# Kernel optimization log

Hardware: AMD Instinct MI355X
Metric: run time of the kernel (lower is better)

## Reference

```python
import jax, jax.numpy as jnp
import numpy as np


def setup_inputs() -> dict:
    key = jax.random.key(0)
    kq, kk, kv = jax.random.split(key, 3)
    B, S, D = 4, 4096, 64
    return {
        "q": jax.random.normal(kq, (B, S, D), dtype=jnp.float32),
        "k": jax.random.normal(kk, (B, S, D), dtype=jnp.float32),
        "v": jax.random.normal(kv, (B, S, D), dtype=jnp.float32),
    }


def reference(q, k, v):
    B, S, D = q.shape
    scale = 1.0 / jnp.sqrt(jnp.asarray(D, dtype=q.dtype))
    # (B, S, S) full score matrix, as in the naive torch implementation
    scores = jnp.einsum("bqd,bkd->bqk", q, k) * scale
    causal_mask = jnp.tril(jnp.ones((S, S), dtype=bool))  # True = keep
    scores = jnp.where(causal_mask, scores, -jnp.inf)
    attn = jax.nn.softmax(scores, axis=-1)
    return jnp.einsum("bqk,bkd->bqd", attn, v)
```

## Files before the change

### kernel.cpp

```cpp
#include <hip/hip_runtime.h>
#include <hip/hip_bf16.h>

typedef __bf16 bf16x8 __attribute__((ext_vector_type(8)));
typedef __bf16 bf16x4 __attribute__((ext_vector_type(4)));
typedef float  floatx4 __attribute__((ext_vector_type(4)));

#define SD 4096
#define DH 64
#define NB 4

__device__ __forceinline__ float exp2fast(float x) { return __builtin_amdgcn_exp2f(x); }

__device__ __forceinline__ unsigned pack_bf16_2(float a, float b) {
    union { __bf16 h[2]; unsigned u; } cvt;
    cvt.h[0] = (__bf16)a; cvt.h[1] = (__bf16)b;
    return cvt.u;
}

__device__ __forceinline__ void block_sync_lds() {
    asm volatile("s_waitcnt lgkmcnt(0)\n\ts_barrier" ::: "memory");
}

__global__ __launch_bounds__(256) void prep_kernel(const float* __restrict__ v,
                                                   __bf16* __restrict__ vt) {
    __shared__ __bf16 tile[16][80];
    const int bid = blockIdx.x;
    const int tid = threadIdx.x;
    const int b = bid >> 8, kt = (bid >> 2) & 63, dq = bid & 3;
    {
        int key = tid >> 2, ds = (tid & 3) * 4;
        float4 f = *(const float4*)(v + ((long)b * SD + kt * 64 + key) * DH + dq * 16 + ds);
        tile[ds+0][key] = (__bf16)f.x;
        tile[ds+1][key] = (__bf16)f.y;
        tile[ds+2][key] = (__bf16)f.z;
        tile[ds+3][key] = (__bf16)f.w;
    }
    __syncthreads();
    {
        int dloc = tid >> 4, cs = (tid & 15) * 4;
        bf16x4 o;
#pragma unroll
        for (int i = 0; i < 4; ++i) {
            int col = cs + i;
            int key = ((col >> 5) * 2 + ((col >> 2) & 1)) * 16
                    + ((col >> 3) & 3) * 4 + (col & 3);
            o[i] = tile[dloc][key];
        }
        *(bf16x4*)(vt + ((long)b * DH + dq * 16 + dloc) * SD + kt * 64 + cs) = o;
    }
}

__global__ __launch_bounds__(256, 4) void fa_kernel(const float* __restrict__ q,
                                                    const float* __restrict__ kq,
                                                    const __bf16* __restrict__ vt,
                                                    __bf16* __restrict__ opart,
                                                    float* __restrict__ lpart) {
    __shared__ __bf16 smem[2][8192];

    const int tid  = threadIdx.x;
    const int wave = tid >> 6;
    const int lane = tid & 63;
    const int c    = lane & 15;
    const int quad = lane >> 4;
    const int bid   = blockIdx.x;
    const int batch = bid & 3;
    const int pr    = (bid >> 2) & 31;
    const int qr    = bid >> 7;
    const float sc = 0.125f * 1.4426950408889634f;

    const long offB   = (long)batch * SD * DH;
    const long vtoffB = (long)batch * DH * SD;

    const int krow = tid >> 2, kdc = (tid & 3) * 16;
    auto swz = [](int g) { int row = g >> 3, ch = g & 7; return row * 64 + ((ch ^ (row & 7)) << 3); };
    const int wkA = swz(krow * 8 + (tid & 3) * 2);
    const int wkB = swz(krow * 8 + (tid & 3) * 2 + 1);
    const int gk0 = tid, gk1 = tid + 256;
    const int wv0 = 4096 + swz(gk0), wv1 = 4096 + swz(gk1);
    const int sw   = c & 7;
    const int off0 = ((quad ^ sw) << 3);
    const int off1 = (((quad + 4) ^ sw) << 3);
    const int rowc = c * 64;

#pragma unroll 1
    for (int ph = 0; ph < 2; ++ph) {
        const int T = ph ? 63 - pr : pr;
        const int myq = T * 64 + wave * 16;
        const int qrow = myq + c;

        bf16x8 qf0, qf1;
        {
            const float* qp = q + offB + (long)(myq + c) * DH + quad * 8;
            float4 f0 = *(const float4*)(qp);
            float4 f1 = *(const float4*)(qp + 4);
            float4 f2 = *(const float4*)(qp + 32);
            float4 f3 = *(const float4*)(qp + 36);
            qf0[0]=(__bf16)(f0.x*sc); qf0[1]=(__bf16)(f0.y*sc); qf0[2]=(__bf16)(f0.z*sc); qf0[3]=(__bf16)(f0.w*sc);
            qf0[4]=(__bf16)(f1.x*sc); qf0[5]=(__bf16)(f1.y*sc); qf0[6]=(__bf16)(f1.z*sc); qf0[7]=(__bf16)(f1.w*sc);
            qf1[0]=(__bf16)(f2.x*sc); qf1[1]=(__bf16)(f2.y*sc); qf1[2]=(__bf16)(f2.z*sc); qf1[3]=(__bf16)(f2.w*sc);
            qf1[4]=(__bf16)(f3.x*sc); qf1[5]=(__bf16)(f3.y*sc); qf1[6]=(__bf16)(f3.z*sc); qf1[7]=(__bf16)(f3.w*sc);
        }

        floatx4 o0 = {0.f,0.f,0.f,0.f}, o1 = o0, o2 = o0, o3 = o0;
        float l = 0.0f;

        const int n = (T >= qr) ? ((T - qr) >> 3) + 1 : 0;

        float4 fk0, fk1, fk2, fk3;
        bf16x8 sv0, sv1;
        auto stage = [&](int kt, float4& a0, float4& a1, float4& a2, float4& a3,
                         bf16x8& v0, bf16x8& v1) {
            const float* kg = kq + offB + (long)(kt * 64 + krow) * DH + kdc;
            a0 = *(const float4*)(kg);
            a1 = *(const float4*)(kg + 4);
            a2 = *(const float4*)(kg + 8);
            a3 = *(const float4*)(kg + 12);
            const __bf16* vg = vt + vtoffB + kt * 64;
            v0 = *(const bf16x8*)(vg + (long)(gk0 >> 3) * SD + (gk0 & 7) * 8);
            v1 = *(const bf16x8*)(vg + (long)(gk1 >> 3) * SD + (gk1 & 7) * 8);
        };

        if (n > 0) stage(qr, fk0, fk1, fk2, fk3, sv0, sv1);
        block_sync_lds();

#pragma unroll 1
        for (int j = 0; j < n; ++j) {
            const int kt = qr + 8 * j;
            float4 nk0, nk1, nk2, nk3; bf16x8 nv0, nv1;
            if (j + 1 < n) stage(kt + 8, nk0, nk1, nk2, nk3, nv0, nv1);
            __bf16* buf = smem[j & 1];
            {
                bf16x8 cA, cB;
                cA[0]=(__bf16)fk0.x; cA[1]=(__bf16)fk0.y; cA[2]=(__bf16)fk0.z; cA[3]=(__bf16)fk0.w;
                cA[4]=(__bf16)fk1.x; cA[5]=(__bf16)fk1.y; cA[6]=(__bf16)fk1.z; cA[7]=(__bf16)fk1.w;
                cB[0]=(__bf16)fk2.x; cB[1]=(__bf16)fk2.y; cB[2]=(__bf16)fk2.z; cB[3]=(__bf16)fk2.w;
                cB[4]=(__bf16)fk3.x; cB[5]=(__bf16)fk3.y; cB[6]=(__bf16)fk3.z; cB[7]=(__bf16)fk3.w;
                *(bf16x8*)(buf + wkA) = cA;
                *(bf16x8*)(buf + wkB) = cB;
                *(bf16x8*)(buf + wv0) = sv0;
                *(bf16x8*)(buf + wv1) = sv1;
            }
            fk0 = nk0; fk1 = nk1; fk2 = nk2; fk3 = nk3; sv0 = nv0; sv1 = nv1;
            block_sync_lds();

            const int kbase = kt * 64;
            if (kbase > myq + 15) continue;

            const __bf16* kbuf = buf;
            const __bf16* vbuf = buf + 4096;
            floatx4 sa[4];
#pragma unroll
            for (int t = 0; t < 4; ++t) {
                bf16x8 ka  = *(const bf16x8*)(kbuf + t * 1024 + rowc + off0);
                bf16x8 kb2 = *(const bf16x8*)(kbuf + t * 1024 + rowc + off1);
                floatx4 a = {0.f,0.f,0.f,0.f};
                a = __builtin_amdgcn_mfma_f32_16x16x32_bf16(ka,  qf0, a, 0, 0, 0);
                a = __builtin_amdgcn_mfma_f32_16x16x32_bf16(kb2, qf1, a, 0, 0, 0);
                sa[t] = a;
            }
            float pe[16];
            if (kbase + 63 > myq) {
#pragma unroll
                for (int t = 0; t < 4; ++t)
#pragma unroll
                    for (int r = 0; r < 4; ++r) {
                        int key = kbase + t*16 + quad*4 + r;
                        pe[t*4+r] = (key <= qrow) ? exp2fast(sa[t][r]) : 0.0f;
                    }
            } else {
#pragma unroll
                for (int t = 0; t < 4; ++t)
#pragma unroll
                    for (int r = 0; r < 4; ++r) pe[t*4+r] = exp2fast(sa[t][r]);
            }
            {
                float s8[8], s4v[4];
#pragma unroll
                for (int i = 0; i < 8; ++i) s8[i] = pe[i] + pe[i+8];
#pragma unroll
                for (int i = 0; i < 4; ++i) s4v[i] = s8[i] + s8[i+4];
                l += (s4v[0] + s4v[2]) + (s4v[1] + s4v[3]);
            }
#pragma unroll
            for (int s = 0; s < 2; ++s) {
                union { unsigned u[4]; bf16x8 f; } bp;
#pragma unroll
                for (int jj = 0; jj < 4; ++jj)
                    bp.u[jj] = pack_bf16_2(pe[8*s + 2*jj], pe[8*s + 2*jj + 1]);
                const int offs = s ? off1 : off0;
                bf16x8 v0 = *(const bf16x8*)(vbuf + 0*1024 + rowc + offs);
                bf16x8 v1 = *(const bf16x8*)(vbuf + 1*1024 + rowc + offs);
                bf16x8 v2 = *(const bf16x8*)(vbuf + 2*1024 + rowc + offs);
                bf16x8 v3 = *(const bf16x8*)(vbuf + 3*1024 + rowc + offs);
                o0 = __builtin_amdgcn_mfma_f32_16x16x32_bf16(v0, bp.f, o0, 0, 0, 0);
                o1 = __builtin_amdgcn_mfma_f32_16x16x32_bf16(v1, bp.f, o1, 0, 0, 0);
                o2 = __builtin_amdgcn_mfma_f32_16x16x32_bf16(v2, bp.f, o2, 0, 0, 0);
                o3 = __builtin_amdgcn_mfma_f32_16x16x32_bf16(v3, bp.f, o3, 0, 0, 0);
            }
        }

        l += __shfl_xor(l, 16);
        l += __shfl_xor(l, 32);

        __bf16* ob = opart + ((long)qr * NB + batch) * (long)(SD * DH) + (long)myq * DH;
        {
            floatx4 ov[4] = {o0, o1, o2, o3};
#pragma unroll
            for (int dt = 0; dt < 4; ++dt) {
                uint2 sO;
                sO.x = pack_bf16_2(ov[dt][0], ov[dt][1]);
                sO.y = pack_bf16_2(ov[dt][2], ov[dt][3]);
                *(uint2*)(ob + c * DH + dt*16 + quad*4) = sO;
            }
        }
        if (quad == 0)
            lpart[((long)qr * NB + batch) * SD + myq + c] = l;
    }
}

__global__ __launch_bounds__(256) void combine_kernel(const __bf16* __restrict__ opart,
                                                      const float* __restrict__ lpart,
                                                      float* __restrict__ out) {
    const long t    = (long)blockIdx.x * 256 + threadIdx.x;
    const long base = t * 4;
    const long qq   = base >> 6;
    float n0 = 0.f, n1 = 0.f, n2 = 0.f, n3 = 0.f, den = 0.f;
#pragma unroll
    for (int qr = 0; qr < 8; ++qr) {
        bf16x4 p = *(const bf16x4*)(opart + ((long)qr << 20) + base);
        n0 += (float)p[0]; n1 += (float)p[1]; n2 += (float)p[2]; n3 += (float)p[3];
        den += lpart[((long)qr << 14) + qq];
    }
    float inv = 1.0f / den;
    float4 o; o.x = n0 * inv; o.y = n1 * inv; o.z = n2 * inv; o.w = n3 * inv;
    *(float4*)(out + base) = o;
}

extern "C" void kernel_launch(void* const* d_in, const int* in_sizes, int n_in,
                              void* d_out, int out_size, void* d_ws, size_t ws_size,
                              hipStream_t stream) {
    const float* q = (const float*)d_in[0];
    const float* k = (const float*)d_in[1];
    const float* v = (const float*)d_in[2];
    float* out = (float*)d_out;
    __bf16* vtb   = (__bf16*)d_ws;
    __bf16* opart = (__bf16*)((char*)d_ws + (4u << 20));
    float*  lpart = (float*)((char*)d_ws + (20u << 20));
    prep_kernel<<<dim3(1024), dim3(256), 0, stream>>>(v, vtb);
    fa_kernel<<<dim3(1024), dim3(256), 0, stream>>>(q, k, vtb, opart, lpart);
    combine_kernel<<<dim3(1024), dim3(256), 0, stream>>>(opart, lpart, out);
}
```

Measured before the change: 94.23 us.

## Stage 128-key tiles per iteration and halve the split-K partition count

Each loop iteration now stages two 64-key K/V sub-tiles (128 keys) into a doubled shared buffer and runs the score/PV body twice per barrier. The key dimension is split into 4 partitions instead of 8, so the attention grid drops to 512 blocks and the combine kernel reads half as many partial outputs. The aim is fewer barriers per key processed and less partial-result traffic. The cost is more registers and LDS per block (occupancy bound lowered to 2) and fewer blocks to spread over the CUs, which may hurt load balance under the causal mask.

```diff
diff --git a/kernel.cpp b/kernel.cpp
--- a/kernel.cpp
+++ b/kernel.cpp
@@ -50,12 +50,12 @@
     }
 }
 
-__global__ __launch_bounds__(256, 4) void fa_kernel(const float* __restrict__ q,
+__global__ __launch_bounds__(256, 2) void fa_kernel(const float* __restrict__ q,
                                                     const float* __restrict__ kq,
                                                     const __bf16* __restrict__ vt,
                                                     __bf16* __restrict__ opart,
                                                     float* __restrict__ lpart) {
-    __shared__ __bf16 smem[2][8192];
+    __shared__ __bf16 smem[2][16384];
 
     const int tid  = threadIdx.x;
     const int wave = tid >> 6;
@@ -73,10 +73,10 @@
 
     const int krow = tid >> 2, kdc = (tid & 3) * 16;
     auto swz = [](int g) { int row = g >> 3, ch = g & 7; return row * 64 + ((ch ^ (row & 7)) << 3); };
-    const int wkA = swz(krow * 8 + (tid & 3) * 2);
-    const int wkB = swz(krow * 8 + (tid & 3) * 2 + 1);
+    const int kg0 = krow * 8 + (tid & 3) * 2;
+    const int wkA = swz(kg0), wkB = swz(kg0 + 1);
     const int gk0 = tid, gk1 = tid + 256;
-    const int wv0 = 4096 + swz(gk0), wv1 = 4096 + swz(gk1);
+    const int wva = swz(gk0), wvb = swz(gk1);
     const int sw   = c & 7;
     const int off0 = ((quad ^ sw) << 3);
     const int off1 = (((quad + 4) ^ sw) << 3);
@@ -104,50 +104,27 @@
         floatx4 o0 = {0.f,0.f,0.f,0.f}, o1 = o0, o2 = o0, o3 = o0;
         float l = 0.0f;
 
-        const int n = (T >= qr) ? ((T - qr) >> 3) + 1 : 0;
-
-        float4 fk0, fk1, fk2, fk3;
-        bf16x8 sv0, sv1;
-        auto stage = [&](int kt, float4& a0, float4& a1, float4& a2, float4& a3,
-                         bf16x8& v0, bf16x8& v1) {
-            const float* kg = kq + offB + (long)(kt * 64 + krow) * DH + kdc;
-            a0 = *(const float4*)(kg);
-            a1 = *(const float4*)(kg + 4);
-            a2 = *(const float4*)(kg + 8);
-            a3 = *(const float4*)(kg + 12);
-            const __bf16* vg = vt + vtoffB + kt * 64;
-            v0 = *(const bf16x8*)(vg + (long)(gk0 >> 3) * SD + (gk0 & 7) * 8);
-            v1 = *(const bf16x8*)(vg + (long)(gk1 >> 3) * SD + (gk1 & 7) * 8);
+        const int last = T >> 1;
+        const int n = (last >= qr) ? ((last - qr) >> 2) + 1 : 0;
+
+        float4 fk[8];
+        bf16x8 sv[4];
+        auto stage = [&](int kt, float4* a, bf16x8* vv) {
+            const float* kg = kq + offB + (long)(kt * 128 + krow) * DH + kdc;
+#pragma unroll
+            for (int i = 0; i < 4; ++i) {
+                a[i]     = *(const float4*)(kg + i * 4);
+                a[i + 4] = *(const float4*)(kg + 64 * DH + i * 4);
+            }
+            const __bf16* vg = vt + vtoffB + kt * 128;
+            vv[0] = *(const bf16x8*)(vg + (long)(gk0 >> 3) * SD + (gk0 & 7) * 8);
+            vv[1] = *(const bf16x8*)(vg + (long)(gk1 >> 3) * SD + (gk1 & 7) * 8);
+            vv[2] = *(const bf16x8*)(vg + (long)(gk0 >> 3) * SD + 64 + (gk0 & 7) * 8);
+            vv[3] = *(const bf16x8*)(vg + (long)(gk1 >> 3) * SD + 64 + (gk1 & 7) * 8);
         };
 
-        if (n > 0) stage(qr, fk0, fk1, fk2, fk3, sv0, sv1);
-        block_sync_lds();
-
-#pragma unroll 1
-        for (int j = 0; j < n; ++j) {
-            const int kt = qr + 8 * j;
-            float4 nk0, nk1, nk2, nk3; bf16x8 nv0, nv1;
-            if (j + 1 < n) stage(kt + 8, nk0, nk1, nk2, nk3, nv0, nv1);
-            __bf16* buf = smem[j & 1];
-            {
-                bf16x8 cA, cB;
-                cA[0]=(__bf16)fk0.x; cA[1]=(__bf16)fk0.y; cA[2]=(__bf16)fk0.z; cA[3]=(__bf16)fk0.w;
-                cA[4]=(__bf16)fk1.x; cA[5]=(__bf16)fk1.y; cA[6]=(__bf16)fk1.z; cA[7]=(__bf16)fk1.w;
-                cB[0]=(__bf16)fk2.x; cB[1]=(__bf16)fk2.y; cB[2]=(__bf16)fk2.z; cB[3]=(__bf16)fk2.w;
-                cB[4]=(__bf16)fk3.x; cB[5]=(__bf16)fk3.y; cB[6]=(__bf16)fk3.z; cB[7]=(__bf16)fk3.w;
-                *(bf16x8*)(buf + wkA) = cA;
-                *(bf16x8*)(buf + wkB) = cB;
-                *(bf16x8*)(buf + wv0) = sv0;
-                *(bf16x8*)(buf + wv1) = sv1;
-            }
-            fk0 = nk0; fk1 = nk1; fk2 = nk2; fk3 = nk3; sv0 = nv0; sv1 = nv1;
-            block_sync_lds();
-
-            const int kbase = kt * 64;
-            if (kbase > myq + 15) continue;
-
-            const __bf16* kbuf = buf;
-            const __bf16* vbuf = buf + 4096;
+        auto body = [&](const __bf16* kbuf, const __bf16* vbuf, int kb) {
+            if (kb > myq + 15) return;
             floatx4 sa[4];
 #pragma unroll
             for (int t = 0; t < 4; ++t) {
@@ -159,12 +136,12 @@
                 sa[t] = a;
             }
             float pe[16];
-            if (kbase + 63 > myq) {
+            if (kb + 63 > myq) {
 #pragma unroll
                 for (int t = 0; t < 4; ++t)
 #pragma unroll
                     for (int r = 0; r < 4; ++r) {
-                        int key = kbase + t*16 + quad*4 + r;
+                        int key = kb + t*16 + quad*4 + r;
                         pe[t*4+r] = (key <= qrow) ? exp2fast(sa[t][r]) : 0.0f;
                     }
             } else {
@@ -197,6 +174,38 @@
                 o2 = __builtin_amdgcn_mfma_f32_16x16x32_bf16(v2, bp.f, o2, 0, 0, 0);
                 o3 = __builtin_amdgcn_mfma_f32_16x16x32_bf16(v3, bp.f, o3, 0, 0, 0);
             }
+        };
+
+        if (n > 0) stage(qr, fk, sv);
+        block_sync_lds();
+
+#pragma unroll 1
+        for (int j = 0; j < n; ++j) {
+            const int kt = qr + 4 * j;
+            float4 nk[8]; bf16x8 nv[4];
+            if (j + 1 < n) stage(kt + 4, nk, nv);
+            __bf16* buf = smem[j & 1];
+#pragma unroll
+            for (int h = 0; h < 2; ++h) {
+                bf16x8 cA, cB;
+                const float4 a0 = fk[h*4+0], a1 = fk[h*4+1], a2 = fk[h*4+2], a3 = fk[h*4+3];
+                cA[0]=(__bf16)a0.x; cA[1]=(__bf16)a0.y; cA[2]=(__bf16)a0.z; cA[3]=(__bf16)a0.w;
+                cA[4]=(__bf16)a1.x; cA[5]=(__bf16)a1.y; cA[6]=(__bf16)a1.z; cA[7]=(__bf16)a1.w;
+                cB[0]=(__bf16)a2.x; cB[1]=(__bf16)a2.y; cB[2]=(__bf16)a2.z; cB[3]=(__bf16)a2.w;
+                cB[4]=(__bf16)a3.x; cB[5]=(__bf16)a3.y; cB[6]=(__bf16)a3.z; cB[7]=(__bf16)a3.w;
+                *(bf16x8*)(buf + h*4096 + wkA) = cA;
+                *(bf16x8*)(buf + h*4096 + wkB) = cB;
+                *(bf16x8*)(buf + 8192 + h*4096 + wva) = sv[h*2+0];
+                *(bf16x8*)(buf + 8192 + h*4096 + wvb) = sv[h*2+1];
+            }
+#pragma unroll
+            for (int i = 0; i < 8; ++i) fk[i] = nk[i];
+#pragma unroll
+            for (int i = 0; i < 4; ++i) sv[i] = nv[i];
+            block_sync_lds();
+
+            body(buf,        buf + 8192,  kt * 128);
+            body(buf + 4096, buf + 12288, kt * 128 + 64);
         }
 
         l += __shfl_xor(l, 16);
@@ -226,7 +235,7 @@
     const long qq   = base >> 6;
     float n0 = 0.f, n1 = 0.f, n2 = 0.f, n3 = 0.f, den = 0.f;
 #pragma unroll
-    for (int qr = 0; qr < 8; ++qr) {
+    for (int qr = 0; qr < 4; ++qr) {
         bf16x4 p = *(const bf16x4*)(opart + ((long)qr << 20) + base);
         n0 += (float)p[0]; n1 += (float)p[1]; n2 += (float)p[2]; n3 += (float)p[3];
         den += lpart[((long)qr << 14) + qq];
@@ -245,8 +254,8 @@
     float* out = (float*)d_out;
     __bf16* vtb   = (__bf16*)d_ws;
     __bf16* opart = (__bf16*)((char*)d_ws + (4u << 20));
-    float*  lpart = (float*)((char*)d_ws + (20u << 20));
+    float*  lpart = (float*)((char*)d_ws + (16u << 20));
     prep_kernel<<<dim3(1024), dim3(256), 0, stream>>>(v, vtb);
-    fa_kernel<<<dim3(1024), dim3(256), 0, stream>>>(q, k, vtb, opart, lpart);
+    fa_kernel<<<dim3(512), dim3(256), 0, stream>>>(q, k, vtb, opart, lpart);
     combine_kernel<<<dim3(1024), dim3(256), 0, stream>>>(opart, lpart, out);
 }
```

After: 93.69 us. Within noise of the previous version (-0.6%).

## Pre-swizzle K/V to bf16 tiles and stage via direct global-to-LDS loads

Applied to the files above, without the earlier changes.

The prep kernel now converts K to bf16 and lays out both K and transposed V as pre-swizzled 64x64 tiles. The attention kernel then copies each tile straight into LDS with global_load_lds, with no register round trip. This removes the per-iteration fp32-to-bf16 conversion of K, the register staging and the LDS stores from the main loop, and halves K read traffic. The cost is extra prep work and a barrier that waits on all outstanding loads, which could expose load latency because prefetch now issues after the barrier.

```diff
diff --git a/kernel.cpp b/kernel.cpp
--- a/kernel.cpp
+++ b/kernel.cpp
@@ -17,42 +17,79 @@
     return cvt.u;
 }
 
-__device__ __forceinline__ void block_sync_lds() {
-    asm volatile("s_waitcnt lgkmcnt(0)\n\ts_barrier" ::: "memory");
-}
-
-__global__ __launch_bounds__(256) void prep_kernel(const float* __restrict__ v,
-                                                   __bf16* __restrict__ vt) {
-    __shared__ __bf16 tile[16][80];
+__device__ __forceinline__ void sync_all() {
+    asm volatile("s_waitcnt vmcnt(0) lgkmcnt(0)\n\ts_barrier" ::: "memory");
+}
+
+__device__ __forceinline__ void load_lds16(const void* g, void* l) {
+    __builtin_amdgcn_global_load_lds(
+        (const __attribute__((address_space(1))) unsigned int*)g,
+        (__attribute__((address_space(3))) unsigned int*)l, 16, 0, 0);
+}
+
+__device__ __forceinline__ int swz8(int g) {
+    int row = g >> 3, ch = g & 7;
+    return row * 64 + ((ch ^ (row & 7)) << 3);
+}
+
+__global__ __launch_bounds__(256) void prep_kernel(const float* __restrict__ k,
+                                                   const float* __restrict__ v,
+                                                   __bf16* __restrict__ kbs,
+                                                   __bf16* __restrict__ vts) {
+    __shared__ __bf16 tile[64][72];
     const int bid = blockIdx.x;
     const int tid = threadIdx.x;
-    const int b = bid >> 8, kt = (bid >> 2) & 63, dq = bid & 3;
+    const long base = (long)bid * 4096;
+
     {
-        int key = tid >> 2, ds = (tid & 3) * 4;
-        float4 f = *(const float4*)(v + ((long)b * SD + kt * 64 + key) * DH + dq * 16 + ds);
-        tile[ds+0][key] = (__bf16)f.x;
-        tile[ds+1][key] = (__bf16)f.y;
-        tile[ds+2][key] = (__bf16)f.z;
-        tile[ds+3][key] = (__bf16)f.w;
+        const float* src = k + base + tid * 16;
+        float4 f0 = *(const float4*)(src);
+        float4 f1 = *(const float4*)(src + 4);
+        float4 f2 = *(const float4*)(src + 8);
+        float4 f3 = *(const float4*)(src + 12);
+        bf16x8 c0, c1;
+        c0[0]=(__bf16)f0.x; c0[1]=(__bf16)f0.y; c0[2]=(__bf16)f0.z; c0[3]=(__bf16)f0.w;
+        c0[4]=(__bf16)f1.x; c0[5]=(__bf16)f1.y; c0[6]=(__bf16)f1.z; c0[7]=(__bf16)f1.w;
+        c1[0]=(__bf16)f2.x; c1[1]=(__bf16)f2.y; c1[2]=(__bf16)f2.z; c1[3]=(__bf16)f2.w;
+        c1[4]=(__bf16)f3.x; c1[5]=(__bf16)f3.y; c1[6]=(__bf16)f3.z; c1[7]=(__bf16)f3.w;
+        __bf16* dst = kbs + base;
+        *(bf16x8*)(dst + swz8(tid * 2))     = c0;
+        *(bf16x8*)(dst + swz8(tid * 2 + 1)) = c1;
+    }
+    {
+        int r = tid >> 2, ds0 = (tid & 3) * 16;
+#pragma unroll
+        for (int i = 0; i < 4; ++i) {
+            float4 f = *(const float4*)(v + base + r * 64 + ds0 + i * 4);
+            tile[ds0 + i*4 + 0][r] = (__bf16)f.x;
+            tile[ds0 + i*4 + 1][r] = (__bf16)f.y;
+            tile[ds0 + i*4 + 2][r] = (__bf16)f.z;
+            tile[ds0 + i*4 + 3][r] = (__bf16)f.w;
+        }
     }
     __syncthreads();
     {
-        int dloc = tid >> 4, cs = (tid & 15) * 4;
-        bf16x4 o;
-#pragma unroll
-        for (int i = 0; i < 4; ++i) {
-            int col = cs + i;
-            int key = ((col >> 5) * 2 + ((col >> 2) & 1)) * 16
-                    + ((col >> 3) & 3) * 4 + (col & 3);
-            o[i] = tile[dloc][key];
-        }
-        *(bf16x4*)(vt + ((long)b * DH + dq * 16 + dloc) * SD + kt * 64 + cs) = o;
+        __bf16* dst = vts + base;
+#pragma unroll
+        for (int h = 0; h < 2; ++h) {
+            int qc = tid * 2 + h;
+            int d = qc >> 3, c8 = (qc & 7) * 8;
+            bf16x8 o;
+#pragma unroll
+            for (int i = 0; i < 8; ++i) {
+                int col = c8 + i;
+                int key = ((col >> 5) * 2 + ((col >> 2) & 1)) * 16
+                        + ((col >> 3) & 3) * 4 + (col & 3);
+                o[i] = tile[d][key];
+            }
+            *(bf16x8*)(dst + swz8(qc)) = o;
+        }
     }
 }
 
 __global__ __launch_bounds__(256, 4) void fa_kernel(const float* __restrict__ q,
-                                                    const float* __restrict__ kq,
-                                                    const __bf16* __restrict__ vt,
+                                                    const __bf16* __restrict__ kbs,
+                                                    const __bf16* __restrict__ vts,
                                                     __bf16* __restrict__ opart,
                                                     float* __restrict__ lpart) {
     __shared__ __bf16 smem[2][8192];
@@ -68,19 +105,24 @@
     const int qr    = bid >> 7;
     const float sc = 0.125f * 1.4426950408889634f;
 
-    const long offB   = (long)batch * SD * DH;
-    const long vtoffB = (long)batch * DH * SD;
-
-    const int krow = tid >> 2, kdc = (tid & 3) * 16;
-    auto swz = [](int g) { int row = g >> 3, ch = g & 7; return row * 64 + ((ch ^ (row & 7)) << 3); };
-    const int wkA = swz(krow * 8 + (tid & 3) * 2);
-    const int wkB = swz(krow * 8 + (tid & 3) * 2 + 1);
-    const int gk0 = tid, gk1 = tid + 256;
-    const int wv0 = 4096 + swz(gk0), wv1 = 4096 + swz(gk1);
+    const long offB = (long)batch * SD * DH;
+
     const int sw   = c & 7;
     const int off0 = ((quad ^ sw) << 3);
     const int off1 = (((quad + 4) ^ sw) << 3);
     const int rowc = c * 64;
+
+    const long tileB = (long)batch * 64;
+
+    auto stage = [&](int kt, int bufi) {
+        const char* gsrc = (wave < 2)
+            ? (const char*)(kbs + (tileB + kt) * 4096) + wave * 4096
+            : (const char*)(vts + (tileB + kt) * 4096) + (wave - 2) * 4096;
+        char* ldst = (char*)(&smem[bufi][0]) + wave * 4096;
+#pragma unroll
+        for (int i = 0; i < 4; ++i)
+            load_lds16(gsrc + i * 1024 + lane * 16, ldst + i * 1024);
+    };
 
 #pragma unroll 1
     for (int ph = 0; ph < 2; ++ph) {
@@ -106,48 +148,20 @@
 
         const int n = (T >= qr) ? ((T - qr) >> 3) + 1 : 0;
 
-        float4 fk0, fk1, fk2, fk3;
-        bf16x8 sv0, sv1;
-        auto stage = [&](int kt, float4& a0, float4& a1, float4& a2, float4& a3,
-                         bf16x8& v0, bf16x8& v1) {
-            const float* kg = kq + offB + (long)(kt * 64 + krow) * DH + kdc;
-            a0 = *(const float4*)(kg);
-            a1 = *(const float4*)(kg + 4);
-            a2 = *(const float4*)(kg + 8);
-            a3 = *(const float4*)(kg + 12);
-            const __bf16* vg = vt + vtoffB + kt * 64;
-            v0 = *(const bf16x8*)(vg + (long)(gk0 >> 3) * SD + (gk0 & 7) * 8);
-            v1 = *(const bf16x8*)(vg + (long)(gk1 >> 3) * SD + (gk1 & 7) * 8);
-        };
-
-        if (n > 0) stage(qr, fk0, fk1, fk2, fk3, sv0, sv1);
-        block_sync_lds();
+        sync_all();
+        if (n > 0) stage(qr, 0);
 
 #pragma unroll 1
         for (int j = 0; j < n; ++j) {
             const int kt = qr + 8 * j;
-            float4 nk0, nk1, nk2, nk3; bf16x8 nv0, nv1;
-            if (j + 1 < n) stage(kt + 8, nk0, nk1, nk2, nk3, nv0, nv1);
-            __bf16* buf = smem[j & 1];
-            {
-                bf16x8 cA, cB;
-                cA[0]=(__bf16)fk0.x; cA[1]=(__bf16)fk0.y; cA[2]=(__bf16)fk0.z; cA[3]=(__bf16)fk0.w;
-                cA[4]=(__bf16)fk1.x; cA[5]=(__bf16)fk1.y; cA[6]=(__bf16)fk1.z; cA[7]=(__bf16)fk1.w;
-                cB[0]=(__bf16)fk2.x; cB[1]=(__bf16)fk2.y; cB[2]=(__bf16)fk2.z; cB[3]=(__bf16)fk2.w;
-                cB[4]=(__bf16)fk3.x; cB[5]=(__bf16)fk3.y; cB[6]=(__bf16)fk3.z; cB[7]=(__bf16)fk3.w;
-                *(bf16x8*)(buf + wkA) = cA;
-                *(bf16x8*)(buf + wkB) = cB;
-                *(bf16x8*)(buf + wv0) = sv0;
-                *(bf16x8*)(buf + wv1) = sv1;
-            }
-            fk0 = nk0; fk1 = nk1; fk2 = nk2; fk3 = nk3; sv0 = nv0; sv1 = nv1;
-            block_sync_lds();
+            sync_all();
+            if (j + 1 < n) stage(kt + 8, (j + 1) & 1);
 
             const int kbase = kt * 64;
             if (kbase > myq + 15) continue;
 
-            const __bf16* kbuf = buf;
-            const __bf16* vbuf = buf + 4096;
+            const __bf16* kbuf = &smem[j & 1][0];
+            const __bf16* vbuf = kbuf + 4096;
             floatx4 sa[4];
 #pragma unroll
             for (int t = 0; t < 4; ++t) {
@@ -243,10 +257,11 @@
     const float* k = (const float*)d_in[1];
     const float* v = (const float*)d_in[2];
     float* out = (float*)d_out;
-    __bf16* vtb   = (__bf16*)d_ws;
+    __bf16* kbs   = (__bf16*)d_ws;
+    __bf16* vts   = (__bf16*)((char*)d_ws + (2u << 20));
     __bf16* opart = (__bf16*)((char*)d_ws + (4u << 20));
     float*  lpart = (float*)((char*)d_ws + (20u << 20));
-    prep_kernel<<<dim3(1024), dim3(256), 0, stream>>>(v, vtb);
-    fa_kernel<<<dim3(1024), dim3(256), 0, stream>>>(q, k, vtb, opart, lpart);
+    prep_kernel<<<dim3(256), dim3(256), 0, stream>>>(k, v, kbs, vts);
+    fa_kernel<<<dim3(1024), dim3(256), 0, stream>>>(q, kbs, vts, opart, lpart);
     combine_kernel<<<dim3(1024), dim3(256), 0, stream>>>(opart, lpart, out);
 }
```

Measured after the change: 91.42 us, median of 2. 3.0% less time.
